# Performance work log

Hardware: AMD Instinct MI355X
Metric: run time of the kernel (lower is better)

## Reference

```python
import jax, jax.numpy as jnp
import numpy as np

B, C, CK, HW = 4, 512, 512, 64
EPS = 1e-5


def conv1x1(x, w, b):
    # 1x1 conv == per-pixel linear: x [b,c,h,w], w [o,c], b [o]
    return jnp.einsum('bchw,oc->bohw', x, w) + b[None, :, None, None]


def mean_variance_norm(feat):
    # torch .var(dim=2) defaults to unbiased (ddof=1)
    b, c = feat.shape[:2]
    flat = feat.reshape(b, c, -1)
    mean = flat.mean(axis=-1)
    std = jnp.sqrt(flat.var(axis=-1, ddof=1) + EPS)
    return (feat - mean[:, :, None, None]) / std[:, :, None, None]


def setup_inputs() -> dict:
    key = jax.random.key(0)
    ks = jax.random.split(key, 10)
    sc_k = 1.0 / np.sqrt(CK)
    sc_c = 1.0 / np.sqrt(C)
    return {
        'content': jax.random.normal(ks[0], (B, C, HW, HW), jnp.float32),
        'style': jax.random.normal(ks[1], (B, C, HW, HW), jnp.float32),
        'content_key': jax.random.normal(ks[2], (B, CK, HW, HW), jnp.float32),
        'style_key': jax.random.normal(ks[3], (B, CK, HW, HW), jnp.float32),
        'f_w': jax.random.normal(ks[4], (CK, CK), jnp.float32) * sc_k,
        'f_b': jnp.zeros((CK,), jnp.float32),
        'g_w': jax.random.normal(ks[5], (CK, CK), jnp.float32) * sc_k,
        'g_b': jnp.zeros((CK,), jnp.float32),
        'h_w': jax.random.normal(ks[6], (C, C), jnp.float32) * sc_c,
        'h_b': jnp.zeros((C,), jnp.float32),
        'w_mix': jnp.ones((2,), jnp.float32),
    }


def reference(content, style, content_key, style_key,
              f_w, f_b, g_w, g_b, h_w, h_b, w_mix):
    Fm = conv1x1(content_key, f_w, f_b)   # [b,ck,h,w]
    Gm = conv1x1(style_key, g_w, g_b)     # [b,ck,hs,ws]
    Hm = conv1x1(style, h_w, h_b)         # [b,c,hs,ws]
    b, ck, h, w = Fm.shape
    c = Hm.shape[1]

    G = Gm.reshape(b, ck, -1)                                # [b,ck,Ns]
    style_flat = Hm.reshape(b, c, -1).transpose(0, 2, 1)      # [b,Ns,c]
    Fq = Fm.reshape(b, ck, -1).transpose(0, 2, 1)             # [b,Nc,ck]

    raw_attn = jnp.einsum('bnk,bkm->bnm', Fq, G)              # [b,Nc,Ns]
    attn_dense = jax.nn.softmax(raw_attn, axis=-1)
    attn_sparse = jax.nn.softmax(jax.nn.relu(raw_attn), axis=-1)

    wts = jax.nn.softmax(w_mix)  # exp(w)/sum(exp(w))
    S = jax.nn.softmax(attn_dense * wts[0] + attn_sparse * wts[1], axis=-1)

    mean = jnp.einsum('bnm,bmc->bnc', S, style_flat)          # E[x]
    second = jnp.einsum('bnm,bmc->bnc', S, style_flat ** 2)   # E[x^2]
    std = jnp.sqrt(jax.nn.relu(second - mean ** 2))

    mean = mean.reshape(b, h, w, c).transpose(0, 3, 1, 2)
    std = std.reshape(b, h, w, c).transpose(0, 3, 1, 2)
    return std * mean_variance_norm(content) + mean
```

## Files before the change

### kernel.cpp

```cpp
#include <hip/hip_runtime.h>
#include <hip/hip_bf16.h>
#include <hip/hip_fp16.h>
#include <stdint.h>

typedef float f32x4 __attribute__((ext_vector_type(4)));
typedef short short8 __attribute__((ext_vector_type(8)));
typedef unsigned short ushort4_t __attribute__((ext_vector_type(4)));
typedef unsigned short u16;

static __device__ __forceinline__ u16 f2bf(float f) {
    __hip_bfloat16 h = __float2bfloat16(f);
    return *reinterpret_cast<const u16*>(&h);
}
static __device__ __forceinline__ u16 f2h(float f) {
    __half h = __float2half(f);
    return *reinterpret_cast<const u16*>(&h);
}
static __device__ __forceinline__ float h2f(u16 b) {
    __half h = *reinterpret_cast<const __half*>(&b);
    return __half2float(h);
}

static __device__ __forceinline__ void gload16(const void* g, void* l) {
    __builtin_amdgcn_global_load_lds((const __attribute__((address_space(1))) void*)g,
                                     (__attribute__((address_space(3))) void*)l, 16, 0, 0);
}

__global__ void k_cast3(const float* __restrict__ a, const float* __restrict__ b,
                        const float* __restrict__ c, u16* __restrict__ oa,
                        u16* __restrict__ ob, u16* __restrict__ oc) {
    int i = blockIdx.x * blockDim.x + threadIdx.x;
    int which = i >> 16, j = i & 65535;
    const float* in = (which == 0) ? a : (which == 1) ? b : c;
    u16* out = (which == 0) ? oa : (which == 1) ? ob : oc;
    float4 v = ((const float4*)in)[j];
    ushort4 o;
    o.x = f2bf(v.x); o.y = f2bf(v.y); o.z = f2bf(v.z); o.w = f2bf(v.w);
    ((ushort4*)out)[j] = o;
}

__global__ __launch_bounds__(256) void k_transpose(const float* __restrict__ in, u16* __restrict__ out) {
    __shared__ float t[64][65];
    int b = blockIdx.z;
    int c0 = blockIdx.y * 64;
    int n0 = blockIdx.x * 64;
    const float* ip = in + ((size_t)b * 512 + c0) * 4096 + n0;
#pragma unroll
    for (int i = 0; i < 16; ++i) {
        int idx = threadIdx.x + i * 256;
        int cl = idx >> 6, nl = idx & 63;
        t[cl][nl] = ip[(size_t)cl * 4096 + nl];
    }
    __syncthreads();
    u16* op = out + ((size_t)b * 4096 + n0) * 512 + c0;
#pragma unroll
    for (int i = 0; i < 16; ++i) {
        int idx = threadIdx.x + i * 256;
        int nr = idx >> 6, cc = idx & 63;
        op[(size_t)nr * 512 + cc] = f2bf(t[cc][nr]);
    }
}

__global__ __launch_bounds__(256) void k_cstats(const float* __restrict__ content, float* __restrict__ cstat) {
    int c = blockIdx.x, b = blockIdx.y;
    const float4* r4 = (const float4*)(content + ((size_t)b * 512 + c) * 4096);
    float s = 0.f, ss = 0.f;
    for (int i = threadIdx.x; i < 1024; i += 256) {
        float4 v = r4[i];
        s += v.x + v.y + v.z + v.w;
        ss += v.x * v.x + v.y * v.y + v.z * v.z + v.w * v.w;
    }
#pragma unroll
    for (int k = 1; k < 64; k <<= 1) { s += __shfl_xor(s, k); ss += __shfl_xor(ss, k); }
    __shared__ float ls[4], lss[4];
    int w = threadIdx.x >> 6;
    if ((threadIdx.x & 63) == 0) { ls[w] = s; lss[w] = ss; }
    __syncthreads();
    if (threadIdx.x == 0) {
        s = ls[0] + ls[1] + ls[2] + ls[3];
        ss = lss[0] + lss[1] + lss[2] + lss[3];
        float mu = s / 4096.f;
        float var = (ss - 4096.f * mu * mu) / 4095.f;
        cstat[((size_t)b * 512 + c) * 2] = mu;
        cstat[((size_t)b * 512 + c) * 2 + 1] = rsqrtf(var + 1e-5f);
    }
}

__global__ __launch_bounds__(256) void k_convP(const u16* __restrict__ XT, const u16* __restrict__ Wb,
                                               const float* __restrict__ bias, u16* __restrict__ out) {
    int bid = blockIdx.x;
    int b = (bid & 7) >> 1;
    int u = ((bid & 1) << 8) | (bid >> 3);
    int n0 = (u & 63) * 64, o0 = (u >> 6) * 64;
    int lane = threadIdx.x & 63, w = threadIdx.x >> 6;
    int l15 = lane & 15, l4 = lane >> 4;
    const u16* ap = XT + ((size_t)b * 4096 + n0 + w * 16 + l15) * 512 + l4 * 8;
    f32x4 acc[4] = {{0,0,0,0},{0,0,0,0},{0,0,0,0},{0,0,0,0}};
#pragma unroll
    for (int kk = 0; kk < 16; ++kk) {
        short8 a = *(const short8*)(ap + kk * 32);
#pragma unroll
        for (int bo = 0; bo < 4; ++bo) {
            const u16* bp = Wb + ((size_t)(o0 + bo * 16 + l15)) * 512 + kk * 32 + l4 * 8;
            short8 bb = *(const short8*)bp;
            acc[bo] = __builtin_amdgcn_mfma_f32_16x16x32_bf16(a, bb, acc[bo], 0, 0, 0);
        }
    }
#pragma unroll
    for (int bo = 0; bo < 4; ++bo) {
        float bv = bias[o0 + bo * 16 + l15];
#pragma unroll
        for (int r = 0; r < 4; ++r) {
            int n = n0 + w * 16 + l4 * 4 + r;
            out[((size_t)b * 4096 + n) * 512 + o0 + bo * 16 + l15] = f2bf(acc[bo][r] + bv);
        }
    }
}

__global__ __launch_bounds__(256) void k_convH(const u16* __restrict__ ST, const u16* __restrict__ Wb,
                                               const float* __restrict__ bias, u16* __restrict__ out) {
    int bid = blockIdx.x;
    int b = (bid & 7) >> 1;
    int u = ((bid & 1) << 8) | (bid >> 3);
    int m0 = (u & 63) * 64, o0 = (u >> 6) * 64;
    int lane = threadIdx.x & 63, w = threadIdx.x >> 6;
    int l15 = lane & 15, l4 = lane >> 4;
    const u16* ap = Wb + ((size_t)(o0 + w * 16 + l15)) * 512 + l4 * 8;
    f32x4 acc[4] = {{0,0,0,0},{0,0,0,0},{0,0,0,0},{0,0,0,0}};
#pragma unroll
    for (int kk = 0; kk < 16; ++kk) {
        short8 a = *(const short8*)(ap + kk * 32);
#pragma unroll
        for (int mb = 0; mb < 4; ++mb) {
            const u16* bp = ST + ((size_t)b * 4096 + m0 + mb * 16 + l15) * 512 + kk * 32 + l4 * 8;
            short8 bb = *(const short8*)bp;
            acc[mb] = __builtin_amdgcn_mfma_f32_16x16x32_bf16(a, bb, acc[mb], 0, 0, 0);
        }
    }
#pragma unroll
    for (int r = 0; r < 4; ++r) {
        int o = o0 + w * 16 + l4 * 4 + r;
        float bv = bias[o];
#pragma unroll
        for (int mb = 0; mb < 4; ++mb) {
            float v = acc[mb][r] + bv;
            size_t base = ((size_t)b * 1024 + o) * 4096 + m0 + mb * 16 + l15;
            out[base] = f2bf(v);
            out[base + (size_t)512 * 4096] = f2bf(v * v);
        }
    }
}

__global__ __launch_bounds__(512, 4) void k_attnA(
    const u16* __restrict__ Q, const u16* __restrict__ G,
    u16* __restrict__ Lg, float* __restrict__ stats) {

    __shared__ __align__(16) u16 gtile[2][32 * 512];
    __shared__ float smd[4][2][16], ssd_[4][2][16], smsp[4][2][16], sssp[4][2][16];

    int bid = blockIdx.x;
    int b = (bid & 7) >> 1;
    int half = bid & 1;
    int qt = bid >> 3;
    int n0 = qt * 64;
    int kv0 = half * 2048;
    int lane = threadIdx.x & 63, w = threadIdx.x >> 6;
    int l15 = lane & 15, l4 = lane >> 4;
    int R = w >> 1, MB = w & 1;

    const u16* qp = Q + ((size_t)b * 4096 + n0 + R * 16 + l15) * 512 + l4 * 8;
    short8 q[16];
#pragma unroll
    for (int kk = 0; kk < 16; ++kk) q[kk] = *(const short8*)(qp + kk * 32);

    const char* gbat = (const char*)(G + (size_t)b * 4096 * 512);
    size_t lgoff = ((size_t)b * 4096 + n0 + R * 16 + l15) * 4096 + kv0 + MB * 16 + l4 * 4;

#define STAGEA(buf, mc)                                                                \
    {                                                                                  \
        _Pragma("unroll")                                                              \
        for (int j = 0; j < 4; ++j) {                                                  \
            int row = j * 8 + w;                                                       \
            const char* src = gbat + ((size_t)(kv0 + (mc) * 32 + row)) * 1024          \
                              + ((lane * 16) ^ ((row & 7) << 4));                      \
            gload16(src, (char*)&gtile[buf][0] + row * 1024);                          \
        }                                                                              \
    }

    float md = -1e30f, sd = 0.f, ms = -1e30f, ss = 0.f;

    STAGEA(0, 0);
    __syncthreads();
    for (int mc = 0; mc < 64; ++mc) {
        int buf = mc & 1;
        if (mc < 63) STAGEA(buf ^ 1, mc + 1);
        f32x4 acc = {0, 0, 0, 0};
        const char* gt = (const char*)&gtile[buf][0];
        int row = MB * 16 + l15;
#pragma unroll
        for (int kk = 0; kk < 16; ++kk) {
            int y = (kk * 64 + l4 * 16) ^ ((row & 7) << 4);
            short8 gg = *(const short8*)(gt + row * 1024 + y);
            acc = __builtin_amdgcn_mfma_f32_16x16x32_bf16(gg, q[kk], acc, 0, 0, 0);
        }
        float v0 = acc[0], v1 = acc[1], v2 = acc[2], v3 = acc[3];
        float mx = fmaxf(fmaxf(v0, v1), fmaxf(v2, v3));
        float mn = fmaxf(md, mx);
        sd = sd * __expf(md - mn) +
             ((__expf(v0 - mn) + __expf(v1 - mn)) + (__expf(v2 - mn) + __expf(v3 - mn)));
        md = mn;
        float mns = fmaxf(ms, fmaxf(mx, 0.f));
        ss = ss * __expf(ms - mns) +
             ((__expf(fmaxf(v0, 0.f) - mns) + __expf(fmaxf(v1, 0.f) - mns)) +
              (__expf(fmaxf(v2, 0.f) - mns) + __expf(fmaxf(v3, 0.f) - mns)));
        ms = mns;
        ushort4_t pk = {f2h(v0), f2h(v1), f2h(v2), f2h(v3)};
        *(ushort4_t*)(Lg + lgoff + (size_t)mc * 32) = pk;
        __syncthreads();
    }

#pragma unroll
    for (int k = 16; k < 64; k <<= 1) {
        float mo = __shfl_xor(md, k), so = __shfl_xor(sd, k);
        float mn = fmaxf(md, mo);
        sd = sd * __expf(md - mn) + so * __expf(mo - mn);
        md = mn;
        mo = __shfl_xor(ms, k); so = __shfl_xor(ss, k);
        mn = fmaxf(ms, mo);
        ss = ss * __expf(ms - mn) + so * __expf(mo - mn);
        ms = mn;
    }
    if (l4 == 0) {
        smd[R][MB][l15] = md; ssd_[R][MB][l15] = sd;
        smsp[R][MB][l15] = ms; sssp[R][MB][l15] = ss;
    }
    __syncthreads();
    if (MB == 0 && lane < 16) {
        float m0_ = smd[R][0][l15], s0_ = ssd_[R][0][l15];
        float m1_ = smd[R][1][l15], s1_ = ssd_[R][1][l15];
        float mn = fmaxf(m0_, m1_);
        float Sd = s0_ * __expf(m0_ - mn) + s1_ * __expf(m1_ - mn);
        float Md = mn;
        m0_ = smsp[R][0][l15]; s0_ = sssp[R][0][l15];
        m1_ = smsp[R][1][l15]; s1_ = sssp[R][1][l15];
        mn = fmaxf(m0_, m1_);
        float Ss = s0_ * __expf(m0_ - mn) + s1_ * __expf(m1_ - mn);
        float Ms = mn;
        int qg = n0 + R * 16 + l15;
        float4 st = {Md, Sd, Ms, Ss};
        *(float4*)(stats + (((size_t)b * 4096 + qg) * 2 + half) * 4) = st;
    }
#undef STAGEA
}

__global__ __launch_bounds__(512, 4) void k_attnB(
    const u16* __restrict__ Lg, const u16* __restrict__ H,
    const float* __restrict__ stats, const float* __restrict__ wmix,
    const float* __restrict__ content, const float* __restrict__ cstat,
    float* __restrict__ out) {

    __shared__ __align__(16) u16 et[2][4096];
    __shared__ float zrow[64];

    int bid = blockIdx.x;
    int b = (bid & 7) >> 1;
    int cs = bid & 1;
    int qt = bid >> 3;
    int n0 = qt * 64;
    int lane = threadIdx.x & 63, w = threadIdx.x >> 6;
    int l15 = lane & 15, l4 = lane >> 4;

    float wa = wmix[0], wbv = wmix[1];
    float wmx = fmaxf(wa, wbv);
    float e0 = __expf(wa - wmx), e1 = __expf(wbv - wmx);
    float w0 = e0 / (e0 + e1), w1 = e1 / (e0 + e1);

    int qlocal = w * 8 + (lane >> 3);
    int kvl = (lane & 7) * 8;
    float md, isd, ms, iss;
    {
        const float* sp = stats + (((size_t)b * 4096 + n0 + qlocal) * 2) * 4;
        float4 s0 = *(const float4*)sp;
        float4 s1 = *(const float4*)(sp + 4);
        float mn = fmaxf(s0.x, s1.x);
        float S = s0.y * __expf(s0.x - mn) + s1.y * __expf(s1.x - mn);
        md = mn; isd = 1.f / S;
        mn = fmaxf(s0.z, s1.z);
        S = s0.w * __expf(s0.z - mn) + s1.w * __expf(s1.z - mn);
        ms = mn; iss = 1.f / S;
    }
    const u16* lgrow = Lg + ((size_t)b * 4096 + n0 + qlocal) * 4096 + kvl;
    unsigned ewbyte = (unsigned)(qlocal * 128) + (((unsigned)(lane & 7) * 16) ^ ((unsigned)(qlocal & 7) << 4));

    float z = 0.f;

#define PRODUCE(buf, mc)                                                               \
    {                                                                                  \
        short8 L8 = *(const short8*)(lgrow + (size_t)(mc) * 64);                       \
        short8 ebf;                                                                    \
        _Pragma("unroll")                                                              \
        for (int j = 0; j < 8; ++j) {                                                  \
            float v = h2f((u16)L8[j]);                                                 \
            float ed = __expf(v - md) * isd;                                           \
            float es = __expf(fmaxf(v, 0.f) - ms) * iss;                               \
            float e = __expf(w0 * ed + w1 * es);                                       \
            z += e;                                                                    \
            ebf[j] = (short)f2bf(e);                                                   \
        }                                                                              \
        *(short8*)((char*)&et[buf][0] + ewbyte) = ebf;                                 \
    }

    f32x4 pv[16];
#pragma unroll
    for (int i = 0; i < 16; ++i) pv[i] = (f32x4){0, 0, 0, 0};

    PRODUCE(0, 0);
    __syncthreads();
    for (int mc = 0; mc < 64; ++mc) {
        int buf = mc & 1;
        if (mc < 63) PRODUCE(buf ^ 1, mc + 1);
        const char* eb = (const char*)&et[buf][0];
        const u16* hb = H + (size_t)b * 1024 * 4096 + (size_t)mc * 64 + l4 * 8;
#pragma unroll
        for (int ks = 0; ks < 2; ++ks) {
            short8 af[4];
#pragma unroll
            for (int qf = 0; qf < 4; ++qf) {
                int qq = qf * 16 + l15;
                int y = (ks * 64 + l4 * 16) ^ ((qq & 7) << 4);
                af[qf] = *(const short8*)(eb + qq * 128 + y);
            }
#pragma unroll
            for (int cf = 0; cf < 4; ++cf) {
                int c = (cf < 2) ? (cs * 256 + w * 32 + cf * 16 + l15)
                                 : (512 + cs * 256 + w * 32 + (cf - 2) * 16 + l15);
                short8 hh = *(const short8*)(hb + (size_t)c * 4096 + ks * 32);
#pragma unroll
                for (int qf = 0; qf < 4; ++qf)
                    pv[qf * 4 + cf] = __builtin_amdgcn_mfma_f32_16x16x32_bf16(af[qf], hh, pv[qf * 4 + cf], 0, 0, 0);
            }
        }
        __syncthreads();
    }

    z += __shfl_xor(z, 1);
    z += __shfl_xor(z, 2);
    z += __shfl_xor(z, 4);
    if ((lane & 7) == 0) zrow[qlocal] = z;
    __syncthreads();

#pragma unroll
    for (int qf = 0; qf < 4; ++qf) {
        float iz[4];
#pragma unroll
        for (int r = 0; r < 4; ++r)
            iz[r] = 1.f / zrow[qf * 16 + l4 * 4 + r];
#pragma unroll
        for (int cf = 0; cf < 2; ++cf) {
            int c = cs * 256 + w * 32 + cf * 16 + l15;
            float mu = cstat[((size_t)b * 512 + c) * 2];
            float rstd = cstat[((size_t)b * 512 + c) * 2 + 1];
            const float* cp = content + ((size_t)b * 512 + c) * 4096 + n0 + qf * 16 + l4 * 4;
            float* op = out + ((size_t)b * 512 + c) * 4096 + n0 + qf * 16 + l4 * 4;
            float4 cv = *(const float4*)cp;
            float4 ov;
#pragma unroll
            for (int r = 0; r < 4; ++r) {
                float mean = pv[qf * 4 + cf][r] * iz[r];
                float sec = pv[qf * 4 + cf + 2][r] * iz[r];
                float stdv = sqrtf(fmaxf(sec - mean * mean, 0.f));
                (&ov.x)[r] = stdv * ((&cv.x)[r] - mu) * rstd + mean;
            }
            *(float4*)op = ov;
        }
    }
#undef PRODUCE
}

extern "C" void kernel_launch(void* const* d_in, const int* in_sizes, int n_in,
                              void* d_out, int out_size, void* d_ws, size_t ws_size,
                              hipStream_t stream) {
    (void)in_sizes; (void)n_in; (void)out_size; (void)ws_size;
    const float* content = (const float*)d_in[0];
    const float* style   = (const float*)d_in[1];
    const float* ckey    = (const float*)d_in[2];
    const float* skey    = (const float*)d_in[3];
    const float* f_w = (const float*)d_in[4];
    const float* f_b = (const float*)d_in[5];
    const float* g_w = (const float*)d_in[6];
    const float* g_b = (const float*)d_in[7];
    const float* h_w = (const float*)d_in[8];
    const float* h_b = (const float*)d_in[9];
    const float* wmix = (const float*)d_in[10];
    float* out = (float*)d_out;

    const size_t MiB = 1048576;
    char* ws = (char*)d_ws;
    u16* ckT = (u16*)(ws + 0);
    u16* skT = (u16*)(ws + 16 * MiB);
    u16* stT = (u16*)(ws + 32 * MiB);
    u16* fwB = (u16*)(ws + 48 * MiB);
    u16* gwB = (u16*)(ws + 48 * MiB + 524288);
    u16* hwB = (u16*)(ws + 49 * MiB);
    float* cst = (float*)(ws + 49 * MiB + 524288);
    u16* Qb  = (u16*)(ws + 50 * MiB);
    u16* Gb  = (u16*)(ws + 66 * MiB);
    u16* Hb  = (u16*)(ws + 0);
    u16* Lg  = (u16*)(ws + 82 * MiB);
    float* stats = (float*)(ws + 210 * MiB);

    k_cast3<<<768, 256, 0, stream>>>(f_w, g_w, h_w, fwB, gwB, hwB);
    k_transpose<<<dim3(64, 8, 4), 256, 0, stream>>>(ckey, ckT);
    k_transpose<<<dim3(64, 8, 4), 256, 0, stream>>>(skey, skT);
    k_transpose<<<dim3(64, 8, 4), 256, 0, stream>>>(style, stT);
    k_cstats<<<dim3(512, 4), 256, 0, stream>>>(content, cst);
    k_convP<<<dim3(2048), 256, 0, stream>>>(ckT, fwB, f_b, Qb);
    k_convP<<<dim3(2048), 256, 0, stream>>>(skT, gwB, g_b, Gb);
    k_convH<<<dim3(2048), 256, 0, stream>>>(stT, hwB, h_b, Hb);
    k_attnA<<<dim3(512), 512, 0, stream>>>(Qb, Gb, Lg, stats);
    k_attnB<<<dim3(512), 512, 0, stream>>>(Lg, Hb, stats, wmix, content, cst, out);
}
```

Measured before the change: 760.4 us.

## Enlarge attnB tiles to 128 queries, use exp2 softmax and prefetch logits

attnA now stores logits prescaled by log2(e), and attnB folds max and log-sum into exp2 offsets, so each softmax term costs one exp2 and no multiply. attnB is restructured to 1024-thread blocks covering 128 queries, so each H tile load is reused across twice as many queries. The block-to-tile mapping is also reordered. The logit loads are prefetched one iteration ahead, and setprio raises wave priority around the MFMA section. Halving the grid to 256 blocks with one block per CU may leave some CUs underused, and register pressure at 1024 threads could cause spills.

```diff
diff --git a/kernel.cpp b/kernel.cpp
--- a/kernel.cpp
+++ b/kernel.cpp
@@ -7,6 +7,16 @@
 typedef short short8 __attribute__((ext_vector_type(8)));
 typedef unsigned short ushort4_t __attribute__((ext_vector_type(4)));
 typedef unsigned short u16;
+
+#if defined(__has_builtin)
+#if __has_builtin(__builtin_amdgcn_exp2f)
+#define EXP2(x) __builtin_amdgcn_exp2f(x)
+#else
+#define EXP2(x) exp2f(x)
+#endif
+#else
+#define EXP2(x) exp2f(x)
+#endif
 
 static __device__ __forceinline__ u16 f2bf(float f) {
     __hip_bfloat16 h = __float2bfloat16(f);
@@ -167,6 +177,7 @@
     int lane = threadIdx.x & 63, w = threadIdx.x >> 6;
     int l15 = lane & 15, l4 = lane >> 4;
     int R = w >> 1, MB = w & 1;
+    const float L2E = 1.44269504f;
 
     const u16* qp = Q + ((size_t)b * 4096 + n0 + R * 16 + l15) * 512 + l4 * 8;
     short8 q[16];
@@ -214,7 +225,7 @@
              ((__expf(fmaxf(v0, 0.f) - mns) + __expf(fmaxf(v1, 0.f) - mns)) +
               (__expf(fmaxf(v2, 0.f) - mns) + __expf(fmaxf(v3, 0.f) - mns)));
         ms = mns;
-        ushort4_t pk = {f2h(v0), f2h(v1), f2h(v2), f2h(v3)};
+        ushort4_t pk = {f2h(v0 * L2E), f2h(v1 * L2E), f2h(v2 * L2E), f2h(v3 * L2E)};
         *(ushort4_t*)(Lg + lgoff + (size_t)mc * 32) = pk;
         __syncthreads();
     }
@@ -253,72 +264,84 @@
 #undef STAGEA
 }
 
-__global__ __launch_bounds__(512, 4) void k_attnB(
+__global__ __launch_bounds__(1024, 1) void k_attnB(
     const u16* __restrict__ Lg, const u16* __restrict__ H,
     const float* __restrict__ stats, const float* __restrict__ wmix,
     const float* __restrict__ content, const float* __restrict__ cstat,
     float* __restrict__ out) {
 
-    __shared__ __align__(16) u16 et[2][4096];
-    __shared__ float zrow[64];
+    __shared__ __align__(16) u16 et[2][8192];
+    __shared__ float zrow[128];
 
     int bid = blockIdx.x;
     int b = (bid & 7) >> 1;
-    int cs = bid & 1;
-    int qt = bid >> 3;
-    int n0 = qt * 64;
-    int lane = threadIdx.x & 63, w = threadIdx.x >> 6;
+    int qt = ((bid & 1) << 4) | (bid >> 4);
+    int cs = (bid >> 3) & 1;
+    int n0 = qt * 128;
+    int tid = threadIdx.x;
+    int lane = tid & 63, w = tid >> 6;
     int l15 = lane & 15, l4 = lane >> 4;
-
+    int qh = w & 1, chw = w >> 1;
+
+    const float L2E = 1.44269504f;
     float wa = wmix[0], wbv = wmix[1];
     float wmx = fmaxf(wa, wbv);
     float e0 = __expf(wa - wmx), e1 = __expf(wbv - wmx);
-    float w0 = e0 / (e0 + e1), w1 = e1 / (e0 + e1);
-
-    int qlocal = w * 8 + (lane >> 3);
-    int kvl = (lane & 7) * 8;
-    float md, isd, ms, iss;
+    float w0l = e0 / (e0 + e1) * L2E, w1l = e1 / (e0 + e1) * L2E;
+
+    int prow = tid >> 3;
+    int kvb = (tid & 7) * 8;
+    float md2, ms2;
     {
-        const float* sp = stats + (((size_t)b * 4096 + n0 + qlocal) * 2) * 4;
+        const float* sp = stats + (((size_t)b * 4096 + n0 + prow) * 2) * 4;
         float4 s0 = *(const float4*)sp;
         float4 s1 = *(const float4*)(sp + 4);
         float mn = fmaxf(s0.x, s1.x);
         float S = s0.y * __expf(s0.x - mn) + s1.y * __expf(s1.x - mn);
-        md = mn; isd = 1.f / S;
+        md2 = mn * L2E + __log2f(S);
         mn = fmaxf(s0.z, s1.z);
         S = s0.w * __expf(s0.z - mn) + s1.w * __expf(s1.z - mn);
-        ms = mn; iss = 1.f / S;
-    }
-    const u16* lgrow = Lg + ((size_t)b * 4096 + n0 + qlocal) * 4096 + kvl;
-    unsigned ewbyte = (unsigned)(qlocal * 128) + (((unsigned)(lane & 7) * 16) ^ ((unsigned)(qlocal & 7) << 4));
-
+        ms2 = mn * L2E + __log2f(S);
+    }
+    const u16* lgrow = Lg + ((size_t)b * 4096 + n0 + prow) * 4096 + kvb;
+    unsigned ewbyte = (unsigned)(prow * 128) +
+                      (((unsigned)(tid & 7) * 16) ^ ((unsigned)(prow & 7) << 4));
     float z = 0.f;
 
-#define PRODUCE(buf, mc)                                                               \
+#define PRODUCE(ebase, LV)                                                             \
     {                                                                                  \
-        short8 L8 = *(const short8*)(lgrow + (size_t)(mc) * 64);                       \
+        short8 L8 = (LV);                                                              \
         short8 ebf;                                                                    \
+        float za = 0.f, zb = 0.f;                                                      \
         _Pragma("unroll")                                                              \
         for (int j = 0; j < 8; ++j) {                                                  \
-            float v = h2f((u16)L8[j]);                                                 \
-            float ed = __expf(v - md) * isd;                                           \
-            float es = __expf(fmaxf(v, 0.f) - ms) * iss;                               \
-            float e = __expf(w0 * ed + w1 * es);                                       \
-            z += e;                                                                    \
+            float t = h2f((u16)L8[j]);                                                 \
+            float ed = EXP2(t - md2);                                                  \
+            float es = EXP2(fmaxf(t, 0.f) - ms2);                                      \
+            float e = EXP2(fmaf(w0l, ed, w1l * es));                                   \
+            if (j & 1) zb += e; else za += e;                                          \
             ebf[j] = (short)f2bf(e);                                                   \
         }                                                                              \
-        *(short8*)((char*)&et[buf][0] + ewbyte) = ebf;                                 \
+        z += za + zb;                                                                  \
+        *(short8*)((char*)(ebase) + ewbyte) = ebf;                                     \
     }
 
     f32x4 pv[16];
 #pragma unroll
     for (int i = 0; i < 16; ++i) pv[i] = (f32x4){0, 0, 0, 0};
 
-    PRODUCE(0, 0);
-    __syncthreads();
+    short8 Lcur = *(const short8*)(lgrow);
+    PRODUCE(&et[0][0], Lcur);
+    short8 Lnext = *(const short8*)(lgrow + 64);
+    __syncthreads();
+
     for (int mc = 0; mc < 64; ++mc) {
         int buf = mc & 1;
-        if (mc < 63) PRODUCE(buf ^ 1, mc + 1);
+        if (mc < 63) {
+            short8 Lp = Lnext;
+            if (mc < 62) Lnext = *(const short8*)(lgrow + (size_t)(mc + 2) * 64);
+            PRODUCE(&et[buf ^ 1][0], Lp);
+        }
         const char* eb = (const char*)&et[buf][0];
         const u16* hb = H + (size_t)b * 1024 * 4096 + (size_t)mc * 64 + l4 * 8;
 #pragma unroll
@@ -326,19 +349,21 @@
             short8 af[4];
 #pragma unroll
             for (int qf = 0; qf < 4; ++qf) {
-                int qq = qf * 16 + l15;
+                int qq = qh * 64 + qf * 16 + l15;
                 int y = (ks * 64 + l4 * 16) ^ ((qq & 7) << 4);
                 af[qf] = *(const short8*)(eb + qq * 128 + y);
             }
+            __builtin_amdgcn_s_setprio(1);
 #pragma unroll
             for (int cf = 0; cf < 4; ++cf) {
-                int c = (cf < 2) ? (cs * 256 + w * 32 + cf * 16 + l15)
-                                 : (512 + cs * 256 + w * 32 + (cf - 2) * 16 + l15);
+                int c = (cf < 2) ? (cs * 256 + chw * 32 + cf * 16 + l15)
+                                 : (512 + cs * 256 + chw * 32 + (cf - 2) * 16 + l15);
                 short8 hh = *(const short8*)(hb + (size_t)c * 4096 + ks * 32);
 #pragma unroll
                 for (int qf = 0; qf < 4; ++qf)
                     pv[qf * 4 + cf] = __builtin_amdgcn_mfma_f32_16x16x32_bf16(af[qf], hh, pv[qf * 4 + cf], 0, 0, 0);
             }
+            __builtin_amdgcn_s_setprio(0);
         }
         __syncthreads();
     }
@@ -346,7 +371,7 @@
     z += __shfl_xor(z, 1);
     z += __shfl_xor(z, 2);
     z += __shfl_xor(z, 4);
-    if ((lane & 7) == 0) zrow[qlocal] = z;
+    if ((tid & 7) == 0) zrow[prow] = z;
     __syncthreads();
 
 #pragma unroll
@@ -354,14 +379,14 @@
         float iz[4];
 #pragma unroll
         for (int r = 0; r < 4; ++r)
-            iz[r] = 1.f / zrow[qf * 16 + l4 * 4 + r];
+            iz[r] = 1.f / zrow[qh * 64 + qf * 16 + l4 * 4 + r];
 #pragma unroll
         for (int cf = 0; cf < 2; ++cf) {
-            int c = cs * 256 + w * 32 + cf * 16 + l15;
+            int c = cs * 256 + chw * 32 + cf * 16 + l15;
             float mu = cstat[((size_t)b * 512 + c) * 2];
             float rstd = cstat[((size_t)b * 512 + c) * 2 + 1];
-            const float* cp = content + ((size_t)b * 512 + c) * 4096 + n0 + qf * 16 + l4 * 4;
-            float* op = out + ((size_t)b * 512 + c) * 4096 + n0 + qf * 16 + l4 * 4;
+            const float* cp = content + ((size_t)b * 512 + c) * 4096 + n0 + qh * 64 + qf * 16 + l4 * 4;
+            float* op = out + ((size_t)b * 512 + c) * 4096 + n0 + qh * 64 + qf * 16 + l4 * 4;
             float4 cv = *(const float4*)cp;
             float4 ov;
 #pragma unroll
@@ -418,5 +443,5 @@
     k_convP<<<dim3(2048), 256, 0, stream>>>(skT, gwB, g_b, Gb);
     k_convH<<<dim3(2048), 256, 0, stream>>>(stT, hwB, h_b, Hb);
     k_attnA<<<dim3(512), 512, 0, stream>>>(Qb, Gb, Lg, stats);
-    k_attnB<<<dim3(512), 512, 0, stream>>>(Lg, Hb, stats, wmix, content, cst, out);
-}
+    k_attnB<<<dim3(256), 1024, 0, stream>>>(Lg, Hb, stats, wmix, content, cst, out);
+}
```

After: 811.0 us. 1.07x slower.
